# Performance work log

Hardware: AMD Instinct MI355X
Metric: run time of the kernel (lower is better)

The kernel has to match this reference:

```python
import jax, jax.numpy as jnp
import numpy as np

N_EMBD = 1024
N_HEAD = 16
HEAD_SIZE = N_EMBD // N_HEAD  # 64
BLOCK_SIZE = 2048
HIDDEN = 2 * N_EMBD  # SwiGLU hidden
LN_EPS = 1e-5


def layernorm(x, w, b):
    m = jnp.mean(x, axis=-1, keepdims=True)
    v = jnp.mean(jnp.square(x - m), axis=-1, keepdims=True)
    return (x - m) * jax.lax.rsqrt(v + LN_EPS) * w + b


def rotate_half(x):
    # interleaved halves, exactly as the torch code: stack((-x2, x1)).reshape
    x1 = x[..., 0::2]
    x2 = x[..., 1::2]
    return jnp.stack((-x2, x1), axis=-1).reshape(x.shape)


def rope_tables(T, hd):
    inv_freq = 1.0 / (10000.0 ** (jnp.arange(0, hd, 2, dtype=jnp.float32) / hd))
    t = jnp.arange(T, dtype=jnp.float32)
    freqs = t[:, None] * inv_freq[None, :]           # [T, hd/2]
    emb = jnp.concatenate([freqs, freqs], axis=-1)   # [T, hd]
    return jnp.cos(emb), jnp.sin(emb)


def setup_inputs() -> dict:
    key = jax.random.key(0)
    ks = jax.random.split(key, 12)
    s = 0.02
    d = {
        "x": jax.random.normal(ks[0], (2, BLOCK_SIZE, N_EMBD), dtype=jnp.float32),
        "ln1_w": jnp.ones((N_EMBD,), jnp.float32),
        "ln1_b": jnp.zeros((N_EMBD,), jnp.float32),
        "ln2_w": jnp.ones((N_EMBD,), jnp.float32),
        "ln2_b": jnp.zeros((N_EMBD,), jnp.float32),
        # per-head projections, stored (H, C, hd); equivalent to x @ W.T in torch
        "Wq": jax.random.normal(ks[1], (N_HEAD, N_EMBD, HEAD_SIZE), jnp.float32) * s,
        "Wk": jax.random.normal(ks[2], (N_HEAD, N_EMBD, HEAD_SIZE), jnp.float32) * s,
        "Wv": jax.random.normal(ks[3], (N_HEAD, N_EMBD, HEAD_SIZE), jnp.float32) * s,
        "proj_w": jax.random.normal(ks[4], (N_EMBD, N_EMBD), jnp.float32) * s,
        "proj_b": jnp.zeros((N_EMBD,), jnp.float32),
        # SwiGLU MLP
        "w_w": jax.random.normal(ks[5], (N_EMBD, HIDDEN), jnp.float32) * s,
        "w_b": jnp.zeros((HIDDEN,), jnp.float32),
        "v_w": jax.random.normal(ks[6], (N_EMBD, HIDDEN), jnp.float32) * s,
        "v_b": jnp.zeros((HIDDEN,), jnp.float32),
        "p_w": jax.random.normal(ks[7], (HIDDEN, N_EMBD), jnp.float32) * s,
        "p_b": jnp.zeros((N_EMBD,), jnp.float32),
    }
    return d


def reference(x, ln1_w, ln1_b, ln2_w, ln2_b, Wq, Wk, Wv, proj_w, proj_b,
              w_w, w_b, v_w, v_b, p_w, p_b):
    B, T, C = x.shape
    # --- attention sub-block ---
    h = layernorm(x, ln1_w, ln1_b)
    q = jnp.einsum('btc,hcd->bhtd', h, Wq)
    k = jnp.einsum('btc,hcd->bhtd', h, Wk)
    v = jnp.einsum('btc,hcd->bhtd', h, Wv)
    cos, sin = rope_tables(T, HEAD_SIZE)  # [T, hd]
    cos = cos[None, None]
    sin = sin[None, None]
    q = q * cos + rotate_half(q) * sin
    k = k * cos + rotate_half(k) * sin
    scale = 1.0 / jnp.sqrt(jnp.float32(HEAD_SIZE))
    scores = jnp.einsum('bhtd,bhsd->bhts', q, k) * scale  # [B,H,T,T]
    causal = jnp.tril(jnp.ones((T, T), dtype=bool))
    scores = jnp.where(causal[None, None], scores, -jnp.inf)
    att = jax.nn.softmax(scores, axis=-1)
    o = jnp.einsum('bhts,bhsd->bhtd', att, v)
    o = o.transpose(0, 2, 1, 3).reshape(B, T, C)  # concat heads
    sa = o @ proj_w + proj_b
    x = x + sa
    # --- SwiGLU FFN sub-block ---
    h2 = layernorm(x, ln2_w, ln2_b)
    a = h2 @ w_w + w_b
    a = a * jax.nn.sigmoid(a)  # swish
    b = h2 @ v_w + v_b
    ff = (a * b) @ p_w + p_b
    return x + ff
```

## Files before the change

kernel.cpp:

```cpp
#include <hip/hip_runtime.h>
#include <math.h>

#define N_EMBD    1024
#define N_HEAD    16
#define HEAD_SIZE 64
#define T_SEQ     2048
#define BATCH     2
#define HIDDEN    2048
#define ROWS      4096

typedef __attribute__((ext_vector_type(8))) short bf16x8;
typedef __attribute__((ext_vector_type(4))) float f32x4;
typedef __attribute__((ext_vector_type(16))) float f32x16;
typedef unsigned short u16;

__device__ __forceinline__ u16 f2bf(float x) {
    union { float f; unsigned u; } v; v.f = x;
    unsigned r = v.u + 0x7fffu + ((v.u >> 16) & 1u);
    return (u16)(r >> 16);
}
__device__ __forceinline__ float bf2f(u16 h) {
    union { unsigned u; float f; } v; v.u = ((unsigned)h) << 16;
    return v.f;
}
__device__ __forceinline__ unsigned cvtpk_bf16(float lo, float hi) {
    unsigned r;
    asm volatile("v_cvt_pk_bf16_f32 %0, %1, %2" : "=v"(r) : "v"(lo), "v"(hi));
    return r;
}
__device__ __forceinline__ void gload16(const void* g, void* lds) {
    __builtin_amdgcn_global_load_lds((const __attribute__((address_space(1))) void*)g,
                                     (__attribute__((address_space(3))) void*)lds, 16, 0, 0);
}

__device__ __forceinline__ void wtrans_body(const float* s, u16* d, int ldS, int ldD,
                                            int k0, int n0, float Ts[64][65])
{
    const int tid = threadIdx.x;
    const int rr = tid >> 4, c4 = (tid & 15) * 4;
#pragma unroll
    for (int i = 0; i < 4; i++) {
        float4 v = *(const float4*)(s + (size_t)(k0 + rr + i * 16) * ldS + n0 + c4);
        Ts[rr + i * 16][c4 + 0] = v.x;
        Ts[rr + i * 16][c4 + 1] = v.y;
        Ts[rr + i * 16][c4 + 2] = v.z;
        Ts[rr + i * 16][c4 + 3] = v.w;
    }
    __syncthreads();
    const int nr = tid >> 2, kc = (tid & 3) * 16;
#pragma unroll
    for (int j = 0; j < 4; j++) {
        u16 t0 = f2bf(Ts[kc + j * 4 + 0][nr]);
        u16 t1 = f2bf(Ts[kc + j * 4 + 1][nr]);
        u16 t2 = f2bf(Ts[kc + j * 4 + 2][nr]);
        u16 t3 = f2bf(Ts[kc + j * 4 + 3][nr]);
        *(ushort4*)(d + (size_t)(n0 + nr) * ldD + k0 + kc + j * 4) = make_ushort4(t0, t1, t2, t3);
    }
}

__global__ __launch_bounds__(256) void wtrans(const float* __restrict__ src, u16* __restrict__ dst,
                                              int ldS, int ldD)
{
    __shared__ float Ts[64][65];
    wtrans_body(src, dst, ldS, ldD, blockIdx.x * 64, blockIdx.y * 64, Ts);
}

__global__ __launch_bounds__(256) void wtrans_qkv(const float* __restrict__ Wq, const float* __restrict__ Wk,
                                                  const float* __restrict__ Wv, u16* __restrict__ dst)
{
    __shared__ float Ts[64][65];
    const int z = blockIdx.z;
    const int which = z >> 4;
    const float* s = (which == 0 ? Wq : (which == 1 ? Wk : Wv)) + (size_t)(z & 15) * 65536;
    wtrans_body(s, dst + (size_t)z * 65536, HEAD_SIZE, N_EMBD, blockIdx.x * 64, 0, Ts);
}

__global__ __launch_bounds__(256) void wtrans_wv(const float* __restrict__ ww, const float* __restrict__ vv,
                                                 u16* __restrict__ dw, u16* __restrict__ dv)
{
    __shared__ float Ts[64][65];
    const int z = blockIdx.z;
    const float* s = (z >> 5) ? vv : ww;
    u16* d = (z >> 5) ? dv : dw;
    wtrans_body(s, d, HIDDEN, N_EMBD, blockIdx.x * 64, (z & 31) * 64, Ts);
}

__global__ __launch_bounds__(256) void ln_kernel(const float* __restrict__ x,
                                                 const float* __restrict__ w,
                                                 const float* __restrict__ b,
                                                 u16* __restrict__ out)
{
    const int row = blockIdx.x;
    const int tid = threadIdx.x;
    const float* xr = x + (size_t)row * N_EMBD;
    float4 v = *(const float4*)(xr + tid * 4);
    float s  = v.x + v.y + v.z + v.w;
    float s2 = v.x*v.x + v.y*v.y + v.z*v.z + v.w*v.w;
#pragma unroll
    for (int off = 32; off; off >>= 1) {
        s  += __shfl_xor(s, off);
        s2 += __shfl_xor(s2, off);
    }
    __shared__ float ss[4], ss2[4];
    if ((tid & 63) == 0) { ss[tid >> 6] = s; ss2[tid >> 6] = s2; }
    __syncthreads();
    s  = ss[0] + ss[1] + ss[2] + ss[3];
    s2 = ss2[0] + ss2[1] + ss2[2] + ss2[3];
    const float mean = s * (1.0f / N_EMBD);
    const float var  = s2 * (1.0f / N_EMBD) - mean * mean;
    const float rstd = rsqrtf(var + 1e-5f);
    float4 wv = *(const float4*)(w + tid * 4);
    float4 bv = *(const float4*)(b + tid * 4);
    ushort4 st = make_ushort4(f2bf((v.x - mean) * rstd * wv.x + bv.x),
                              f2bf((v.y - mean) * rstd * wv.y + bv.y),
                              f2bf((v.z - mean) * rstd * wv.z + bv.z),
                              f2bf((v.w - mean) * rstd * wv.w + bv.w));
    *(ushort4*)(out + (size_t)row * N_EMBD + tid * 4) = st;
}

__global__ __launch_bounds__(256) void rope_kernel(u16* __restrict__ q, u16* __restrict__ k)
{
    const int u = blockIdx.x * 256 + threadIdx.x;
    const int i  = u & 31;
    const int t  = (u >> 5) & (T_SEQ - 1);
    const int bh = u >> 16;
    const size_t base = ((size_t)bh * T_SEQ + t) * HEAD_SIZE + 2 * i;
    const float L = 0.28782313662425572f;
    const int i0 = (2 * i) & 31, i1 = (2 * i + 1) & 31;
    float c0, s0, c1, s1;
    sincosf((float)t * __expf(-(float)i0 * L), &s0, &c0);
    sincosf((float)t * __expf(-(float)i1 * L), &s1, &c1);
    float a0 = bf2f(q[base]), a1 = bf2f(q[base + 1]);
    q[base]     = f2bf(a0 * c0 - a1 * s0);
    q[base + 1] = f2bf(a1 * c1 + a0 * s1);
    float b0 = bf2f(k[base]), b1 = bf2f(k[base + 1]);
    k[base]     = f2bf(b0 * c0 - b1 * s0);
    k[base + 1] = f2bf(b1 * c1 + b0 * s1);
}

__global__ __launch_bounds__(256) void gemm_br(const u16* __restrict__ A, const u16* __restrict__ Bt,
                                               const float* __restrict__ bias, const float* __restrict__ resid,
                                               float* __restrict__ Cf,
                                               int N, int K)
{
    __shared__ __align__(16) u16 As[2][128 * 64];
    __shared__ __align__(16) u16 Bs[2][64 * 64];
    const int tid = threadIdx.x, w = tid >> 6, l = tid & 63, l15 = l & 15, l4 = l >> 4;
    const int wm = w >> 1, wn = w & 1;
    const int n0 = blockIdx.x * 64, m0 = blockIdx.y * 128;
    f32x4 acc[4][2] = {};
    const int NT = K >> 6;

    auto stage = [&](int buf, int k0) {
#pragma unroll
        for (int c = 0; c < 4; c++) {
            const int slot = c * 256 + tid;
            const int row = slot >> 3;
            const int sw = ((slot & 7) * 16) ^ ((row & 7) << 4);
            gload16((const char*)(A + (size_t)(m0 + row) * K + k0) + sw, (char*)&As[buf][0] + slot * 16);
        }
#pragma unroll
        for (int c = 0; c < 2; c++) {
            const int slot = c * 256 + tid;
            const int row = slot >> 3;
            const int sw = ((slot & 7) * 16) ^ ((row & 7) << 4);
            gload16((const char*)(Bt + (size_t)(n0 + row) * K + k0) + sw, (char*)&Bs[buf][0] + slot * 16);
        }
    };

    stage(0, 0);
    __syncthreads();
    int cur = 0;
    for (int t = 0; t < NT; t++) {
        if (t + 1 < NT) stage(cur ^ 1, (t + 1) << 6);
#pragma unroll
        for (int ks = 0; ks < 2; ks++) {
            const int cb = ks * 64 + l4 * 16;
            bf16x8 af[4], bf[2];
#pragma unroll
            for (int mt = 0; mt < 4; mt++) {
                const int row = wm * 64 + mt * 16 + l15;
                af[mt] = *(const bf16x8*)((const char*)&As[cur][0] + row * 128 + (cb ^ ((row & 7) << 4)));
            }
#pragma unroll
            for (int u = 0; u < 2; u++) {
                const int row = wn * 32 + u * 16 + l15;
                bf[u] = *(const bf16x8*)((const char*)&Bs[cur][0] + row * 128 + (cb ^ ((row & 7) << 4)));
            }
#pragma unroll
            for (int mt = 0; mt < 4; mt++)
#pragma unroll
                for (int u = 0; u < 2; u++)
                    acc[mt][u] = __builtin_amdgcn_mfma_f32_16x16x32_bf16(af[mt], bf[u], acc[mt][u], 0, 0, 0);
        }
        __syncthreads();
        cur ^= 1;
    }
#pragma unroll
    for (int mt = 0; mt < 4; mt++) {
#pragma unroll
        for (int u = 0; u < 2; u++) {
            const int n = n0 + wn * 32 + u * 16 + l15;
            const float bi = bias[n];
#pragma unroll
            for (int r = 0; r < 4; r++) {
                const int m = m0 + wm * 64 + mt * 16 + l4 * 4 + r;
                const size_t idx = (size_t)m * N + n;
                Cf[idx] = acc[mt][u][r] + bi + resid[idx];
            }
        }
    }
}

__global__ __launch_bounds__(256, 4) void gemm_qkv(const u16* __restrict__ A, const u16* __restrict__ Bt,
                                                   u16* __restrict__ qo, u16* __restrict__ ko, u16* __restrict__ vto)
{
    __shared__ __align__(16) u16 As[2][64 * 64];
    __shared__ __align__(16) u16 Bs[2][64 * 64];
    const int tid = threadIdx.x, w = tid >> 6, l = tid & 63, l15 = l & 15, l4 = l >> 4;
    const int wm = w >> 1, wn = w & 1;
    const int n0 = blockIdx.x * 128, m0 = blockIdx.y * 128;
    const int K = N_EMBD;
    f32x4 acc[4][4] = {};
    const int NT = K >> 5;

    auto stage = [&](int buf, int k0) {
#pragma unroll
        for (int c = 0; c < 2; c++) {
            const int slot = c * 256 + tid;
            const int r2 = slot >> 3;
            const int w16u = (slot & 7) ^ (r2 & 7);
            const int grow = (w16u >> 2) * 64 + r2;
            const int kc = w16u & 3;
            gload16(A  + (size_t)(m0 + grow) * K + k0 + kc * 8, (char*)&As[buf][0] + slot * 16);
            gload16(Bt + (size_t)(n0 + grow) * K + k0 + kc * 8, (char*)&Bs[buf][0] + slot * 16);
        }
    };

    stage(0, 0);
    __syncthreads();
    int cur = 0;
    for (int t = 0; t < NT; t++) {
        if (t + 1 < NT) stage(cur ^ 1, (t + 1) << 5);
        bf16x8 af[4], bf[4];
#pragma unroll
        for (int q4 = 0; q4 < 4; q4++) {
            const int ga = wm * 64 + q4 * 16 + l15;
            const int ra = ga & 63, ha = ga >> 6;
            af[q4] = *(const bf16x8*)((const char*)&As[cur][0] + ra * 128 + (((ha << 2) | l4) ^ (ra & 7)) * 16);
            const int gb = wn * 64 + q4 * 16 + l15;
            const int rb = gb & 63, hb = gb >> 6;
            bf[q4] = *(const bf16x8*)((const char*)&Bs[cur][0] + rb * 128 + (((hb << 2) | l4) ^ (rb & 7)) * 16);
        }
#pragma unroll
        for (int mt = 0; mt < 4; mt++)
#pragma unroll
            for (int nt = 0; nt < 4; nt++)
                acc[mt][nt] = __builtin_amdgcn_mfma_f32_16x16x32_bf16(af[mt], bf[nt], acc[mt][nt], 0, 0, 0);
        __syncthreads();
        cur ^= 1;
    }
#pragma unroll
    for (int mt = 0; mt < 4; mt++) {
#pragma unroll
        for (int nt = 0; nt < 4; nt++) {
            const int n = n0 + wn * 64 + nt * 16 + l15;
            const int which = n >> 10, hd = (n >> 6) & 15, dd = n & 63;
            const int mb = m0 + wm * 64 + mt * 16 + l4 * 4;
            const int bI = mb >> 11, tq = mb & (T_SEQ - 1);
            if (which == 2) {
                ushort4 st = make_ushort4(f2bf(acc[mt][nt][0]), f2bf(acc[mt][nt][1]),
                                          f2bf(acc[mt][nt][2]), f2bf(acc[mt][nt][3]));
                *(ushort4*)(vto + ((size_t)(bI * N_HEAD + hd) * HEAD_SIZE + dd) * T_SEQ + tq) = st;
            } else {
                u16* dst = (which == 0) ? qo : ko;
#pragma unroll
                for (int r = 0; r < 4; r++)
                    dst[((size_t)(bI * N_HEAD + hd) * T_SEQ + tq + r) * HEAD_SIZE + dd] = f2bf(acc[mt][nt][r]);
            }
        }
    }
}

__global__ __launch_bounds__(256, 4) void gemm_glu(const u16* __restrict__ A, const u16* __restrict__ Bw,
                                                   const u16* __restrict__ Bv,
                                                   const float* __restrict__ wb, const float* __restrict__ vb,
                                                   u16* __restrict__ G)
{
    __shared__ __align__(16) u16 As[2][64 * 64];
    __shared__ __align__(16) u16 Bws[2][32 * 64];
    __shared__ __align__(16) u16 Bvs[2][32 * 64];
    const int tid = threadIdx.x, w = tid >> 6, l = tid & 63, l15 = l & 15, l4 = l >> 4;
    const int wm = w >> 1, wn = w & 1;
    const int n0 = blockIdx.x * 64, m0 = blockIdx.y * 128;
    const int K = N_EMBD;
    f32x4 accA[4][2] = {};
    f32x4 accB[4][2] = {};
    const int NT = K >> 5;

    auto stage = [&](int buf, int k0) {
#pragma unroll
        for (int c = 0; c < 2; c++) {
            const int slot = c * 256 + tid;
            const int r2 = slot >> 3;
            const int w16u = (slot & 7) ^ (r2 & 7);
            const int grow = (w16u >> 2) * 64 + r2;
            const int kc = w16u & 3;
            gload16(A + (size_t)(m0 + grow) * K + k0 + kc * 8, (char*)&As[buf][0] + slot * 16);
        }
        {
            const int slot = tid;
            const int r2 = slot >> 3;
            const int w16u = (slot & 7) ^ (r2 & 7);
            const int grow = (w16u >> 2) * 32 + r2;
            const int kc = w16u & 3;
            gload16(Bw + (size_t)(n0 + grow) * K + k0 + kc * 8, (char*)&Bws[buf][0] + slot * 16);
            gload16(Bv + (size_t)(n0 + grow) * K + k0 + kc * 8, (char*)&Bvs[buf][0] + slot * 16);
        }
    };

    stage(0, 0);
    __syncthreads();
    int cur = 0;
    for (int t = 0; t < NT; t++) {
        if (t + 1 < NT) stage(cur ^ 1, (t + 1) << 5);
        bf16x8 af[4], bwf[2], bvf[2];
#pragma unroll
        for (int q4 = 0; q4 < 4; q4++) {
            const int ga = wm * 64 + q4 * 16 + l15;
            const int ra = ga & 63, ha = ga >> 6;
            af[q4] = *(const bf16x8*)((const char*)&As[cur][0] + ra * 128 + (((ha << 2) | l4) ^ (ra & 7)) * 16);
        }
#pragma unroll
        for (int u = 0; u < 2; u++) {
            const int gb = wn * 32 + u * 16 + l15;
            const int rb = gb & 31, hb = gb >> 5;
            const int off = rb * 128 + (((hb << 2) | l4) ^ (rb & 7)) * 16;
            bwf[u] = *(const bf16x8*)((const char*)&Bws[cur][0] + off);
            bvf[u] = *(const bf16x8*)((const char*)&Bvs[cur][0] + off);
        }
#pragma unroll
        for (int mt = 0; mt < 4; mt++)
#pragma unroll
            for (int u = 0; u < 2; u++) {
                accA[mt][u] = __builtin_amdgcn_mfma_f32_16x16x32_bf16(af[mt], bwf[u], accA[mt][u], 0, 0, 0);
                accB[mt][u] = __builtin_amdgcn_mfma_f32_16x16x32_bf16(af[mt], bvf[u], accB[mt][u], 0, 0, 0);
            }
        __syncthreads();
        cur ^= 1;
    }
#pragma unroll
    for (int mt = 0; mt < 4; mt++) {
#pragma unroll
        for (int u = 0; u < 2; u++) {
            const int n = n0 + wn * 32 + u * 16 + l15;
            const float wbi = wb[n], vbi = vb[n];
#pragma unroll
            for (int r = 0; r < 4; r++) {
                const int m = m0 + wm * 64 + mt * 16 + l4 * 4 + r;
                const float a  = accA[mt][u][r] + wbi;
                const float bb = accB[mt][u][r] + vbi;
                G[(size_t)m * HIDDEN + n] = f2bf(a / (1.f + __expf(-a)) * bb);
            }
        }
    }
}

__global__ __launch_bounds__(256, 4) void attn_mfma(const u16* __restrict__ q, const u16* __restrict__ k,
                                                    const u16* __restrict__ vt, u16* __restrict__ o)
{
    __shared__ __align__(16) u16 Kb[2][64 * 64];
    __shared__ __align__(16) u16 Vb[2][64 * 64];
    __shared__ float ml[2][32];
    const int tid = threadIdx.x, l = tid & 63, l31 = l & 31, hh2 = (l >> 5) & 1;
    const int wid  = tid >> 6;
    const int qsub = wid >> 1;
    const int par  = wid & 1;
    const int bh  = blockIdx.x;
    const int qtb = (int)gridDim.y - 1 - (int)blockIdx.y;
    const int qt  = qtb * 2 + qsub;
    const int qw0 = qt * 32;
    const int nc  = qtb + 1;
    const u16* qb  = q  + (size_t)bh * T_SEQ * HEAD_SIZE;
    const u16* kbg = k  + (size_t)bh * T_SEQ * HEAD_SIZE;
    const u16* vbg = vt + (size_t)bh * HEAD_SIZE * T_SEQ;

    bf16x8 qf[4];
    {
        const u16* qr = qb + (size_t)(qw0 + l31) * HEAD_SIZE + hh2 * 8;
#pragma unroll
        for (int kk = 0; kk < 4; kk++) qf[kk] = *(const bf16x8*)(qr + kk * 16);
    }

    f32x16 oacc0 = {}, oacc1 = {};
    float lrow = 0.f;
    const float qs = 0.125f * 1.44269504088896f;
    const float M0 = 20.f;

    auto stage = [&](int buf, int s0) {
#pragma unroll
        for (int c = 0; c < 2; c++) {
            const int slot = c * 256 + tid;
            const int row = slot >> 3;
            const int sw = ((slot & 7) * 16) ^ ((row & 7) << 4);
            gload16((const char*)(kbg + (size_t)(s0 + row) * HEAD_SIZE) + sw, (char*)&Kb[buf][0] + slot * 16);
        }
#pragma unroll
        for (int c = 0; c < 2; c++) {
            const int slot = c * 256 + tid;
            const int row = slot >> 3;
            const int sw = ((slot & 7) * 16) ^ ((row & 7) << 4);
            gload16((const char*)(vbg + (size_t)row * T_SEQ + s0) + sw, (char*)&Vb[buf][0] + slot * 16);
        }
    };

    stage(0, 0);
    __syncthreads();
    int cur = 0;

    for (int j = 0; j < nc; j++) {
        if (j + 1 < nc) stage(cur ^ 1, (j + 1) * 64);

        const int hc = 2 * j + par;
        if (hc <= qt) {
            f32x16 sa = {};
            const int row = par * 32 + l31;
            const int swz = (row & 7) << 4;
#pragma unroll
            for (int kk = 0; kk < 4; kk++) {
                const bf16x8 kf = *(const bf16x8*)((const char*)&Kb[cur][0] + row * 128 + ((kk * 32 + hh2 * 16) ^ swz));
                sa = __builtin_amdgcn_mfma_f32_32x32x16_bf16(kf, qf[kk], sa, 0, 0, 0);
            }
            if (hc == qt) {
#pragma unroll
                for (int reg = 0; reg < 16; reg++) {
                    const int R = (reg & 3) + 8 * (reg >> 2) + 4 * hh2;
                    if (R > l31) sa[reg] = -1e30f;
                }
            }
            float ls = 0.f;
#pragma unroll
            for (int reg = 0; reg < 16; reg++) {
                const float pv = exp2f(fmaf(sa[reg], qs, -M0));
                sa[reg] = pv;
                ls += pv;
            }
            ls += __shfl_xor(ls, 32);
            lrow += ls;

            unsigned pk[8];
#pragma unroll
            for (int jj = 0; jj < 8; jj++) pk[jj] = cvtpk_bf16(sa[2 * jj], sa[2 * jj + 1]);

#pragma unroll
            for (int st = 0; st < 2; st++) {
                const int b = st * 4;
                union { unsigned u[4]; bf16x8 v; } r;
                const unsigned s0w = (unsigned)__shfl_xor((int)pk[b + 0], 32);
                const unsigned s1w = (unsigned)__shfl_xor((int)pk[b + 1], 32);
                const unsigned s2w = (unsigned)__shfl_xor((int)pk[b + 2], 32);
                const unsigned s3w = (unsigned)__shfl_xor((int)pk[b + 3], 32);
                r.u[0] = hh2 ? s2w : pk[b + 0];
                r.u[1] = hh2 ? s3w : pk[b + 1];
                r.u[2] = hh2 ? pk[b + 2] : s0w;
                r.u[3] = hh2 ? pk[b + 3] : s1w;
#pragma unroll
                for (int dt = 0; dt < 2; dt++) {
                    const int vrow = dt * 32 + l31;
                    const int vswz = (vrow & 7) << 4;
                    const int vcol = (par * 64 + st * 32 + hh2 * 16) ^ vswz;
                    const bf16x8 vf = *(const bf16x8*)((const char*)&Vb[cur][0] + vrow * 128 + vcol);
                    if (dt == 0) oacc0 = __builtin_amdgcn_mfma_f32_32x32x16_bf16(vf, r.v, oacc0, 0, 0, 0);
                    else         oacc1 = __builtin_amdgcn_mfma_f32_32x32x16_bf16(vf, r.v, oacc1, 0, 0, 0);
                }
            }
        }
        __syncthreads();
        cur ^= 1;
    }

    float* obuf = (float*)&Kb[0][0] + (size_t)qsub * 2048;
    if (par == 1) {
#pragma unroll
        for (int reg = 0; reg < 16; reg++) {
            const int R = (reg & 3) + 8 * (reg >> 2) + 4 * hh2;
            obuf[R * 32 + l31] = oacc0[reg];
            obuf[(32 + R) * 32 + l31] = oacc1[reg];
        }
        if (hh2 == 0) ml[qsub][l31] = lrow;
    }
    __syncthreads();
    if (par == 0) {
        const float inv = 1.f / (lrow + ml[qsub][l31]);
        const int bI = bh >> 4, hd = bh & 15;
        u16* ob = o + ((size_t)(bI * T_SEQ + qw0 + l31)) * N_EMBD + hd * HEAD_SIZE;
#pragma unroll
        for (int g = 0; g < 4; g++) {
            const int d0a = g * 8 + hh2 * 4;
            float v0[4], v1[4];
#pragma unroll
            for (int r = 0; r < 4; r++) {
                const int R = d0a + r;
                v0[r] = (oacc0[4 * g + r] + obuf[R * 32 + l31]) * inv;
                v1[r] = (oacc1[4 * g + r] + obuf[(32 + R) * 32 + l31]) * inv;
            }
            *(ushort4*)(ob + d0a)      = make_ushort4(f2bf(v0[0]), f2bf(v0[1]), f2bf(v0[2]), f2bf(v0[3]));
            *(ushort4*)(ob + 32 + d0a) = make_ushort4(f2bf(v1[0]), f2bf(v1[1]), f2bf(v1[2]), f2bf(v1[3]));
        }
    }
}

extern "C" void kernel_launch(void* const* d_in, const int* in_sizes, int n_in,
                              void* d_out, int out_size, void* d_ws, size_t ws_size,
                              hipStream_t stream)
{
    (void)in_sizes; (void)n_in; (void)out_size; (void)ws_size;
    const float* x      = (const float*)d_in[0];
    const float* ln1_w  = (const float*)d_in[1];
    const float* ln1_b  = (const float*)d_in[2];
    const float* ln2_w  = (const float*)d_in[3];
    const float* ln2_b  = (const float*)d_in[4];
    const float* Wq     = (const float*)d_in[5];
    const float* Wk     = (const float*)d_in[6];
    const float* Wv     = (const float*)d_in[7];
    const float* proj_w = (const float*)d_in[8];
    const float* proj_b = (const float*)d_in[9];
    const float* w_w    = (const float*)d_in[10];
    const float* w_b    = (const float*)d_in[11];
    const float* v_w    = (const float*)d_in[12];
    const float* v_b    = (const float*)d_in[13];
    const float* p_w    = (const float*)d_in[14];
    const float* p_b    = (const float*)d_in[15];
    float* out = (float*)d_out;

    char* W = (char*)d_ws;
    u16*   Wqkv = (u16*)(W + 0);
    u16*   pwT  = (u16*)(W + 6291456);
    u16*   wwT  = (u16*)(W + 8388608);
    u16*   vvT  = (u16*)(W + 12582912);
    u16*   ppT  = (u16*)(W + 16777216);
    u16*   h    = (u16*)(W + 20971520);
    u16*   qB   = (u16*)(W + 29360128);
    u16*   kB   = (u16*)(W + 37748736);
    u16*   vtB  = (u16*)(W + 46137344);
    u16*   oB   = (u16*)(W + 54525952);
    float* x1   = (float*)(W + 62914560);
    u16*   ga   = qB;

    wtrans_qkv<<<dim3(16, 1, 48), 256, 0, stream>>>(Wq, Wk, Wv, Wqkv);
    wtrans_wv<<<dim3(16, 1, 64), 256, 0, stream>>>(w_w, v_w, wwT, vvT);
    wtrans<<<dim3(16, 16), 256, 0, stream>>>(proj_w, pwT, 1024, 1024);
    wtrans<<<dim3(32, 16), 256, 0, stream>>>(p_w, ppT, 1024, 2048);

    ln_kernel<<<ROWS, 256, 0, stream>>>(x, ln1_w, ln1_b, h);
    gemm_qkv<<<dim3(24, 32), 256, 0, stream>>>(h, Wqkv, qB, kB, vtB);
    rope_kernel<<<(BATCH * N_HEAD * T_SEQ * 32) / 256, 256, 0, stream>>>(qB, kB);
    attn_mfma<<<dim3(BATCH * N_HEAD, T_SEQ / 64), 256, 0, stream>>>(qB, kB, vtB, oB);
    gemm_br<<<dim3(16, 32), 256, 0, stream>>>(oB, pwT, proj_b, x, x1, N_EMBD, N_EMBD);
    ln_kernel<<<ROWS, 256, 0, stream>>>(x1, ln2_w, ln2_b, h);
    gemm_glu<<<dim3(32, 32), 256, 0, stream>>>(h, wwT, vvT, w_b, v_b, ga);
    gemm_br<<<dim3(16, 32), 256, 0, stream>>>(ga, ppT, p_b, x1, out, N_EMBD, HIDDEN);
}
```

Before: 207.6 us.

## Fold softmax scale into RoPE and compute row sums via ones-MFMA

```diff
diff --git a/kernel.cpp b/kernel.cpp
--- a/kernel.cpp
+++ b/kernel.cpp
@@ -126,13 +126,14 @@
     const int bh = u >> 16;
     const size_t base = ((size_t)bh * T_SEQ + t) * HEAD_SIZE + 2 * i;
     const float L = 0.28782313662425572f;
+    const float QS = 0.125f * 1.44269504088896f;
     const int i0 = (2 * i) & 31, i1 = (2 * i + 1) & 31;
     float c0, s0, c1, s1;
     sincosf((float)t * __expf(-(float)i0 * L), &s0, &c0);
     sincosf((float)t * __expf(-(float)i1 * L), &s1, &c1);
     float a0 = bf2f(q[base]), a1 = bf2f(q[base + 1]);
-    q[base]     = f2bf(a0 * c0 - a1 * s0);
-    q[base + 1] = f2bf(a1 * c1 + a0 * s1);
+    q[base]     = f2bf((a0 * c0 - a1 * s0) * QS);
+    q[base + 1] = f2bf((a1 * c1 + a0 * s1) * QS);
     float b0 = bf2f(k[base]), b1 = bf2f(k[base + 1]);
     k[base]     = f2bf(b0 * c0 - b1 * s0);
     k[base + 1] = f2bf(b1 * c1 + b0 * s1);
@@ -391,10 +392,11 @@
 #pragma unroll
         for (int kk = 0; kk < 4; kk++) qf[kk] = *(const bf16x8*)(qr + kk * 16);
     }
-
-    f32x16 oacc0 = {}, oacc1 = {};
-    float lrow = 0.f;
-    const float qs = 0.125f * 1.44269504088896f;
+    bf16x8 onesf;
+#pragma unroll
+    for (int e = 0; e < 8; e++) onesf[e] = (short)0x3F80;
+
+    f32x16 oacc0 = {}, oacc1 = {}, lacc = {};
     const float M0 = 20.f;
 
     auto stage = [&](int buf, int s0) {
@@ -423,7 +425,9 @@
 
         const int hc = 2 * j + par;
         if (hc <= qt) {
-            f32x16 sa = {};
+            f32x16 sa;
+#pragma unroll
+            for (int reg = 0; reg < 16; reg++) sa[reg] = -M0;
             const int row = par * 32 + l31;
             const int swz = (row & 7) << 4;
 #pragma unroll
@@ -438,15 +442,8 @@
                     if (R > l31) sa[reg] = -1e30f;
                 }
             }
-            float ls = 0.f;
-#pragma unroll
-            for (int reg = 0; reg < 16; reg++) {
-                const float pv = exp2f(fmaf(sa[reg], qs, -M0));
-                sa[reg] = pv;
-                ls += pv;
-            }
-            ls += __shfl_xor(ls, 32);
-            lrow += ls;
+#pragma unroll
+            for (int reg = 0; reg < 16; reg++) sa[reg] = exp2f(sa[reg]);
 
             unsigned pk[8];
 #pragma unroll
@@ -464,6 +461,7 @@
                 r.u[1] = hh2 ? s3w : pk[b + 1];
                 r.u[2] = hh2 ? pk[b + 2] : s0w;
                 r.u[3] = hh2 ? pk[b + 3] : s1w;
+                lacc = __builtin_amdgcn_mfma_f32_32x32x16_bf16(onesf, r.v, lacc, 0, 0, 0);
 #pragma unroll
                 for (int dt = 0; dt < 2; dt++) {
                     const int vrow = dt * 32 + l31;
@@ -487,11 +485,11 @@
             obuf[R * 32 + l31] = oacc0[reg];
             obuf[(32 + R) * 32 + l31] = oacc1[reg];
         }
-        if (hh2 == 0) ml[qsub][l31] = lrow;
+        if (hh2 == 0) ml[qsub][l31] = lacc[0];
     }
     __syncthreads();
     if (par == 0) {
-        const float inv = 1.f / (lrow + ml[qsub][l31]);
+        const float inv = 1.f / (lacc[0] + ml[qsub][l31]);
         const int bI = bh >> 4, hd = bh & 15;
         u16* ob = o + ((size_t)(bI * T_SEQ + qw0 + l31)) * N_EMBD + hd * HEAD_SIZE;
 #pragma unroll
```

Result: no change. 206.8 us (-0.4%).
